# Kernel optimization log

Measured on AMD Instinct MI355X. Metric: run time of the kernel, lower is better.

Reference implementation:

```python
import jax, jax.numpy as jnp
import numpy as np

EMBED_DIM = 1024
NUM_HEADS = 16
HEAD_DIM = EMBED_DIM // NUM_HEADS
SCALE = HEAD_DIM ** -0.5


def setup_inputs() -> dict:
    key = jax.random.key(0)
    ks = jax.random.split(key, 5)
    B, N, D = 2, 2048, EMBED_DIM
    std = D ** -0.5
    x = jax.random.normal(ks[0], (B, N, D), dtype=jnp.float32)
    W_qkv = jax.random.normal(ks[1], (D, 3 * D), dtype=jnp.float32) * std
    b_qkv = jnp.zeros((3 * D,), dtype=jnp.float32)
    W_proj = jax.random.normal(ks[2], (D, D), dtype=jnp.float32) * std
    b_proj = jnp.zeros((D,), dtype=jnp.float32)
    return {"x": x, "W_qkv": W_qkv, "b_qkv": b_qkv, "W_proj": W_proj, "b_proj": b_proj}


def reference(x, W_qkv, b_qkv, W_proj, b_proj):
    B, N, D = x.shape
    H, Hd = NUM_HEADS, HEAD_DIM
    qkv = x @ W_qkv + b_qkv                      # (B, N, 3D)
    qkv = qkv.reshape(B, N, 3, H, Hd)
    q = qkv[:, :, 0].transpose(0, 2, 1, 3)       # (B, H, N, Hd)
    k = qkv[:, :, 1].transpose(0, 2, 1, 3)
    v = qkv[:, :, 2].transpose(0, 2, 1, 3)
    attn = jnp.einsum('bhqd,bhkd->bhqk', q, k) * SCALE  # (B, H, N, N)
    attn = jax.nn.softmax(attn, axis=-1)
    out = jnp.einsum('bhqk,bhkd->bhqd', attn, v)        # (B, H, N, Hd)
    out = out.transpose(0, 2, 1, 3).reshape(B, N, D)
    return out @ W_proj + b_proj
```

## Files before the change

### kernel.cpp

```cpp
#include <hip/hip_runtime.h>
#include <stdint.h>

#define BATCH 2
#define NH 16
#define SEQ 2048
#define DIM 1024
#define HD 64
#define MROWS (BATCH*SEQ)

typedef __attribute__((ext_vector_type(8))) _Float16 f16x8;
typedef __attribute__((ext_vector_type(16))) float f32x16;
typedef __attribute__((ext_vector_type(4))) float f32x4;
typedef __attribute__((ext_vector_type(2))) __fp16 fp16x2;
typedef __attribute__((ext_vector_type(4))) short short4v;
typedef __attribute__((ext_vector_type(2))) unsigned uint2v;

__device__ __forceinline__ short f2h(float f) {
  union { _Float16 h; short s; } u;
  u.h = (_Float16)f;
  return u.s;
}

__device__ __forceinline__ float fast_exp2(float x) {
#if __has_builtin(__builtin_amdgcn_exp2f)
  return __builtin_amdgcn_exp2f(x);
#else
  return exp2f(x);
#endif
}

__device__ __forceinline__ unsigned pk2(float a, float b) {
  union { fp16x2 h; unsigned u; } x;
  x.h = __builtin_amdgcn_cvt_pkrtz(a, b);
  return x.u;
}

__device__ __forceinline__ void perm32swap(unsigned &a, unsigned &b) {
#if __has_builtin(__builtin_amdgcn_permlane32_swap)
  uint2v r = __builtin_amdgcn_permlane32_swap(a, b, false, false);
  a = r[0]; b = r[1];
#else
  unsigned as = (unsigned)__shfl_xor((int)a, 32);
  unsigned bs = (unsigned)__shfl_xor((int)b, 32);
  bool lo = ((threadIdx.x & 63) < 32);
  unsigned na = lo ? a : bs;
  unsigned nb = lo ? as : b;
  a = na; b = nb;
#endif
}

__device__ __forceinline__ void async_load16(const void* g, void* l) {
  __builtin_amdgcn_global_load_lds((const __attribute__((address_space(1))) void*)g,
                                   (__attribute__((address_space(3))) void*)l, 16, 0, 0);
}

__global__ __launch_bounds__(256) void k_cvt(const float* __restrict__ in,
                                             short* __restrict__ out, int n4) {
  int i = blockIdx.x * 256 + threadIdx.x;
  if (i >= n4) return;
  float4 v = ((const float4*)in)[i];
  short4v o;
  o[0] = f2h(v.x); o[1] = f2h(v.y); o[2] = f2h(v.z); o[3] = f2h(v.w);
  ((short4v*)out)[i] = o;
}

__global__ __launch_bounds__(256) void k_transpose(const float* __restrict__ in,
                                                   short* __restrict__ out,
                                                   int K, int N) {
  __shared__ float t[32][33];
  int n0 = blockIdx.x * 32, k0 = blockIdx.y * 32;
  int tx = threadIdx.x, ty = threadIdx.y;
  #pragma unroll
  for (int i = 0; i < 32; i += 8)
    t[ty + i][tx] = in[(size_t)(k0 + ty + i) * N + (n0 + tx)];
  __syncthreads();
  #pragma unroll
  for (int i = 0; i < 32; i += 8)
    out[(size_t)(n0 + ty + i) * K + (k0 + tx)] = f2h(t[tx][ty + i]);
}

template <int MODE, int BM>
__global__ __launch_bounds__(256) void k_gemm_bt(
    const short* __restrict__ A, const short* __restrict__ Bt,
    const float* __restrict__ bias,
    short* __restrict__ Qd, short* __restrict__ Kd, short* __restrict__ Vtd,
    float* __restrict__ Cf, int Ncols, int Kdim) {
  constexpr int BN = 128, BK = 64;
  constexpr int RI = BM / 32;
  __shared__ short Al[2][BM * BK];
  __shared__ short Bl[2][BN * BK];
  const int tid = threadIdx.x;
  const int lane = tid & 63;
  const int wid = tid >> 6;
  const int wr = wid >> 1, wc = wid & 1;
  const int lin = blockIdx.y * (int)gridDim.x + blockIdx.x;
  const int xcd = lin & 7, loc = lin >> 3;
  int bx, by;
  if (MODE == 0) { bx = (xcd & 1) * 12 + loc % 12; by = (xcd >> 1) * 8 + loc / 12; }
  else           { bx = loc % 8;                   by = xcd * 8 + loc / 8; }
  const int m0 = by * BM, n0 = bx * BN;
  const int l15 = lane & 15, lk = (lane >> 4) * 8;

  f32x4 acc[RI][4] = {};

  auto stage = [&](int kt, int buf) {
    int k0 = kt * BK;
    #pragma unroll
    for (int i2 = 0; i2 < BM / 32; i2++) {
      int c = i2 * 256 + tid;
      int r = c >> 3, cs = (c & 7) * 8;
      async_load16(A + (size_t)(m0 + r) * Kdim + k0 + (cs ^ ((r & 7) * 8)),
                   &Al[buf][c * 8]);
    }
    #pragma unroll
    for (int i2 = 0; i2 < 4; i2++) {
      int c = i2 * 256 + tid;
      int r = c >> 3, cs = (c & 7) * 8;
      async_load16(Bt + (size_t)(n0 + r) * Kdim + k0 + (cs ^ ((r & 7) * 8)),
                   &Bl[buf][c * 8]);
    }
  };

  auto compute = [&](int buf) {
    f16x8 af[2][RI], bfr[2][4];
    #pragma unroll
    for (int kk = 0; kk < 2; kk++) {
      #pragma unroll
      for (int i = 0; i < RI; i++) {
        int row = wr * (BM / 2) + i * 16 + l15;
        af[kk][i] = *(const f16x8*)&Al[buf][row * 64 + ((kk * 32 + lk) ^ ((row & 7) * 8))];
      }
      #pragma unroll
      for (int j = 0; j < 4; j++) {
        int row = wc * 64 + j * 16 + l15;
        bfr[kk][j] = *(const f16x8*)&Bl[buf][row * 64 + ((kk * 32 + lk) ^ ((row & 7) * 8))];
      }
    }
    __builtin_amdgcn_s_setprio(1);
    #pragma unroll
    for (int i = 0; i < RI; i++)
      #pragma unroll
      for (int j = 0; j < 4; j++) {
        acc[i][j] = __builtin_amdgcn_mfma_f32_16x16x32_f16(af[0][i], bfr[0][j], acc[i][j], 0, 0, 0);
        acc[i][j] = __builtin_amdgcn_mfma_f32_16x16x32_f16(af[1][i], bfr[1][j], acc[i][j], 0, 0, 0);
      }
    __builtin_amdgcn_s_setprio(0);
  };

  stage(0, 0);
  const int NT = Kdim / BK;
  for (int t = 0; t < NT; t++) {
    int cur = t & 1;
    if (t + 1 < NT) {
      stage(t + 1, cur ^ 1);
      if constexpr (BM == 128) asm volatile("s_waitcnt vmcnt(8)" ::: "memory");
      else                     asm volatile("s_waitcnt vmcnt(6)" ::: "memory");
    } else {
      asm volatile("s_waitcnt vmcnt(0)" ::: "memory");
    }
    __builtin_amdgcn_s_barrier();
    __builtin_amdgcn_sched_barrier(0);
    compute(cur);
    __builtin_amdgcn_sched_barrier(0);
    __builtin_amdgcn_s_barrier();
  }

  const int rl = (lane >> 4) * 4;
  if (MODE == 0) {
    #pragma unroll
    for (int j = 0; j < 4; j++) {
      int col = n0 + wc * 64 + j * 16 + l15;
      float bv = bias[col];
      int sec = col >> 10;
      int cc = col & 1023;
      int h = cc >> 6, hd = cc & 63;
      float mul = (sec == 0) ? (0.125f * 1.44269504088896f) : 1.0f;
      #pragma unroll
      for (int i = 0; i < RI; i++) {
        int rowb = m0 + wr * (BM / 2) + i * 16 + rl;
        #pragma unroll
        for (int r = 0; r < 4; r++) {
          int row = rowb + r;
          int b = row >> 11, nr = row & 2047;
          short v = f2h((acc[i][j][r] + bv) * mul);
          size_t bh = (size_t)(b * NH + h);
          size_t base2 = bh * (size_t)(SEQ * HD);
          if (sec == 0) {
            Qd[base2 + (size_t)nr * HD + hd] = v;
          } else if (sec == 1) {
            Kd[base2 + (size_t)(((nr >> 5) * 4 + (hd >> 4)) * 512 +
                                (((hd >> 3) & 1) * 32 + (nr & 31)) * 8 + (hd & 7))] = v;
          } else {
            Vtd[base2 + (size_t)(((nr >> 4) * 2 + (hd >> 5)) * 512 +
                                 (((nr >> 3) & 1) * 32 + (hd & 31)) * 8 + (nr & 7))] = v;
          }
        }
      }
    }
  } else {
    #pragma unroll
    for (int j = 0; j < 4; j++) {
      int col = n0 + wc * 64 + j * 16 + l15;
      float bv = bias[col];
      #pragma unroll
      for (int i = 0; i < RI; i++) {
        int rowb = m0 + wr * (BM / 2) + i * 16 + rl;
        #pragma unroll
        for (int r = 0; r < 4; r++)
          Cf[(size_t)(rowb + r) * Ncols + col] = acc[i][j][r] + bv;
      }
    }
  }
}

#define QBLK 64
#define NKVT (SEQ / 64)

#define PACK8(sv, R0, lsv, OUT) do {                                        \
    float e0_ = fast_exp2((sv)[R0 + 0]), e1_ = fast_exp2((sv)[R0 + 1]);     \
    float e2_ = fast_exp2((sv)[R0 + 2]), e3_ = fast_exp2((sv)[R0 + 3]);     \
    float e4_ = fast_exp2((sv)[R0 + 4]), e5_ = fast_exp2((sv)[R0 + 5]);     \
    float e6_ = fast_exp2((sv)[R0 + 6]), e7_ = fast_exp2((sv)[R0 + 7]);     \
    lsv += ((e0_ + e1_) + (e2_ + e3_)) + ((e4_ + e5_) + (e6_ + e7_));       \
    unsigned u0_ = pk2(e0_, e1_), u1_ = pk2(e2_, e3_);                      \
    unsigned u2_ = pk2(e4_, e5_), u3_ = pk2(e6_, e7_);                      \
    perm32swap(u0_, u2_);                                                   \
    perm32swap(u1_, u3_);                                                   \
    union { unsigned u[4]; f16x8 v; } W_;                                   \
    W_.u[0] = u0_; W_.u[1] = u1_; W_.u[2] = u2_; W_.u[3] = u3_;             \
    OUT = W_.v;                                                             \
  } while (0)

__global__ __launch_bounds__(256) void k_flash(const short* __restrict__ Qd,
                                               const short* __restrict__ KB,
                                               const short* __restrict__ VB,
                                               short* __restrict__ Od) {
  __shared__ float ob[4096];
  __shared__ float lb[128];
  const int tid = threadIdx.x;
  const int lane = tid & 63;
  const int w = tid >> 6;
  const int wq = w >> 1;
  const int kvh = w & 1;
  const int l31 = lane & 31, lh = lane >> 5;
  const int bh = blockIdx.x;
  const int q0 = blockIdx.y * QBLK + wq * 32;
  const size_t base = (size_t)bh * (size_t)(SEQ * HD);

  f16x8 qf[4];
  #pragma unroll
  for (int ds = 0; ds < 4; ds++)
    qf[ds] = *(const f16x8*)(Qd + base + (size_t)(q0 + l31) * HD + ds * 16 + lh * 8);

  const short* kb = KB + base + kvh * 2048 + (size_t)lane * 8;
  const short* vb = VB + base + kvh * 2048 + (size_t)lane * 8;

  f32x16 o[2] = {};
  float lsum = 0.f;

#define LOADK(t, kf) do {                                                   \
    const short* p_ = kb + (size_t)(t) * 4096;                              \
    kf[0] = *(const f16x8*)(p_);                                            \
    kf[1] = *(const f16x8*)(p_ + 512);                                      \
    kf[2] = *(const f16x8*)(p_ + 1024);                                     \
    kf[3] = *(const f16x8*)(p_ + 1536);                                     \
  } while (0)
#define LOADV(t, vf) do {                                                   \
    const short* p_ = vb + (size_t)(t) * 4096;                              \
    vf[0] = *(const f16x8*)(p_);                               \
    vf[1] = *(const f16x8*)(p_ + 512);                         \
    vf[2] = *(const f16x8*)(p_ + 1024);                        \
    vf[3] = *(const f16x8*)(p_ + 1536);                        \
  } while (0)

  auto compute = [&](const f16x8* kf, const f16x8* vf) {
    f32x16 s = {};
    __builtin_amdgcn_s_setprio(1);
    #pragma unroll
    for (int ds = 0; ds < 4; ds++)
      s = __builtin_amdgcn_mfma_f32_32x32x16_f16(kf[ds], qf[ds], s, 0, 0, 0);
    __builtin_amdgcn_s_setprio(0);
    f16x8 p[2];
    PACK8(s, 0, lsum, p[0]); PACK8(s, 8, lsum, p[1]);
    __builtin_amdgcn_s_setprio(1);
    #pragma unroll
    for (int ks = 0; ks < 2; ks++) {
      o[0] = __builtin_amdgcn_mfma_f32_32x32x16_f16(p[ks], vf[ks * 2 + 0], o[0], 0, 0, 0);
      o[1] = __builtin_amdgcn_mfma_f32_32x32x16_f16(p[ks], vf[ks * 2 + 1], o[1], 0, 0, 0);
    }
    __builtin_amdgcn_s_setprio(0);
  };

  f16x8 kA[4], vA[4], kB_[4], vB_[4];
  LOADK(0, kA); LOADV(0, vA);
  for (int t = 0; t < NKVT; t += 2) {
    if (t + 1 < NKVT) { LOADK(t + 1, kB_); LOADV(t + 1, vB_); }
    compute(kA, vA);
    if (t + 2 < NKVT) { LOADK(t + 2, kA); LOADV(t + 2, vA); }
    if (t + 1 < NKVT) compute(kB_, vB_);
  }
#undef LOADK
#undef LOADV

  if (kvh == 1) {
    #pragma unroll
    for (int hdt = 0; hdt < 2; hdt++)
      #pragma unroll
      for (int rq = 0; rq < 4; rq++) {
        f32x4 v4;
        v4[0] = o[hdt][rq * 4 + 0]; v4[1] = o[hdt][rq * 4 + 1];
        v4[2] = o[hdt][rq * 4 + 2]; v4[3] = o[hdt][rq * 4 + 3];
        *(f32x4*)&ob[wq * 2048 + (hdt * 4 + rq) * 256 + lane * 4] = v4;
      }
    lb[wq * 64 + lane] = lsum;
  }
  __syncthreads();
  if (kvh == 0) {
    #pragma unroll
    for (int hdt = 0; hdt < 2; hdt++)
      #pragma unroll
      for (int rq = 0; rq < 4; rq++) {
        f32x4 v4 = *(const f32x4*)&ob[wq * 2048 + (hdt * 4 + rq) * 256 + lane * 4];
        o[hdt][rq * 4 + 0] += v4[0]; o[hdt][rq * 4 + 1] += v4[1];
        o[hdt][rq * 4 + 2] += v4[2]; o[hdt][rq * 4 + 3] += v4[3];
      }
    lsum += lb[wq * 64 + lane];

    lsum += __shfl_xor(lsum, 32);
    float inv = 1.f / lsum;
    const int b = bh >> 4, h = bh & 15;
    #pragma unroll
    for (int reg = 0; reg < 16; reg++) {
      int qrow = (reg & 3) + 8 * (reg >> 2) + 4 * lh;
      float s = __shfl(inv, qrow);
      size_t r0 = (size_t)(b * SEQ + q0 + qrow) * DIM + h * 64;
      Od[r0 + l31]      = f2h(o[0][reg] * s);
      Od[r0 + 32 + l31] = f2h(o[1][reg] * s);
    }
  }
}

extern "C" void kernel_launch(void* const* d_in, const int* in_sizes, int n_in,
                              void* d_out, int out_size, void* d_ws, size_t ws_size,
                              hipStream_t stream) {
  const float* x     = (const float*)d_in[0];
  const float* Wqkv  = (const float*)d_in[1];
  const float* bqkv  = (const float*)d_in[2];
  const float* Wproj = (const float*)d_in[3];
  const float* bproj = (const float*)d_in[4];
  float* out = (float*)d_out;

  char* ws = (char*)d_ws;
  short* x_h    = (short*)(ws);
  short* Wqkv_t = (short*)(ws + ((size_t)8  << 20));
  short* Wproj_t= (short*)(ws + ((size_t)14 << 20));
  short* Qd     = (short*)(ws + ((size_t)16 << 20));
  short* Kd     = (short*)(ws + ((size_t)24 << 20));
  short* Vtd    = (short*)(ws + ((size_t)32 << 20));
  short* Od     = (short*)(ws + ((size_t)40 << 20));

  k_cvt<<<(MROWS * DIM / 4 + 255) / 256, 256, 0, stream>>>(x, x_h, MROWS * DIM / 4);
  dim3 tb(32, 8);
  k_transpose<<<dim3(3 * DIM / 32, DIM / 32), tb, 0, stream>>>(Wqkv, Wqkv_t, DIM, 3 * DIM);
  k_transpose<<<dim3(DIM / 32, DIM / 32), tb, 0, stream>>>(Wproj, Wproj_t, DIM, DIM);
  k_gemm_bt<0, 128><<<dim3(3 * DIM / 128, MROWS / 128), 256, 0, stream>>>(
      x_h, Wqkv_t, bqkv, Qd, Kd, Vtd, nullptr, 3 * DIM, DIM);
  k_flash<<<dim3(BATCH * NH, SEQ / QBLK), 256, 0, stream>>>(Qd, Kd, Vtd, Od);
  k_gemm_bt<1, 64><<<dim3(DIM / 128, MROWS / 64), 256, 0, stream>>>(
      Od, Wproj_t, bproj, nullptr, nullptr, nullptr, out, DIM, DIM);
}
```

Measured before the change: 130.6 us.

## Split KV range across four waves per 32-query block in flash kernel

Each block now processes 32 queries instead of 64, and its four waves each handle a contiguous quarter of the key/value sequence rather than a 2x2 query/KV-half split. Partial outputs and row sums are merged with a two-stage reduction through shared memory. This doubles the block count and halves each wave's serial loop length, at the cost of each block re-reading the full K/V, so total K/V traffic doubles, and of extra barriers in the reduction.

```diff
diff --git a/kernel.cpp b/kernel.cpp
--- a/kernel.cpp
+++ b/kernel.cpp
@@ -213,8 +213,8 @@
   }
 }
 
-#define QBLK 64
-#define NKVT (SEQ / 64)
+#define QBLK 32
+#define NSTEPS 16
 
 #define PACK8(sv, R0, lsv, OUT) do {                                        \
     float e0_ = fast_exp2((sv)[R0 + 0]), e1_ = fast_exp2((sv)[R0 + 1]);     \
@@ -231,6 +231,13 @@
     OUT = W_.v;                                                             \
   } while (0)
 
+#define LOADH(pt, fr) do {                                                  \
+    fr[0] = *(const f16x8*)(pt);                                            \
+    fr[1] = *(const f16x8*)((pt) + 512);                                    \
+    fr[2] = *(const f16x8*)((pt) + 1024);                                   \
+    fr[3] = *(const f16x8*)((pt) + 1536);                                   \
+  } while (0)
+
 __global__ __launch_bounds__(256) void k_flash(const short* __restrict__ Qd,
                                                const short* __restrict__ KB,
                                                const short* __restrict__ VB,
@@ -240,11 +247,9 @@
   const int tid = threadIdx.x;
   const int lane = tid & 63;
   const int w = tid >> 6;
-  const int wq = w >> 1;
-  const int kvh = w & 1;
   const int l31 = lane & 31, lh = lane >> 5;
   const int bh = blockIdx.x;
-  const int q0 = blockIdx.y * QBLK + wq * 32;
+  const int q0 = blockIdx.y * QBLK;
   const size_t base = (size_t)bh * (size_t)(SEQ * HD);
 
   f16x8 qf[4];
@@ -252,26 +257,11 @@
   for (int ds = 0; ds < 4; ds++)
     qf[ds] = *(const f16x8*)(Qd + base + (size_t)(q0 + l31) * HD + ds * 16 + lh * 8);
 
-  const short* kb = KB + base + kvh * 2048 + (size_t)lane * 8;
-  const short* vb = VB + base + kvh * 2048 + (size_t)lane * 8;
+  const short* kp = KB + base + (size_t)(w * NSTEPS) * 2048 + (size_t)lane * 8;
+  const short* vp = VB + base + (size_t)(w * NSTEPS) * 2048 + (size_t)lane * 8;
 
   f32x16 o[2] = {};
   float lsum = 0.f;
-
-#define LOADK(t, kf) do {                                                   \
-    const short* p_ = kb + (size_t)(t) * 4096;                              \
-    kf[0] = *(const f16x8*)(p_);                                            \
-    kf[1] = *(const f16x8*)(p_ + 512);                                      \
-    kf[2] = *(const f16x8*)(p_ + 1024);                                     \
-    kf[3] = *(const f16x8*)(p_ + 1536);                                     \
-  } while (0)
-#define LOADV(t, vf) do {                                                   \
-    const short* p_ = vb + (size_t)(t) * 4096;                              \
-    vf[0] = *(const f16x8*)(p_);                               \
-    vf[1] = *(const f16x8*)(p_ + 512);                         \
-    vf[2] = *(const f16x8*)(p_ + 1024);                        \
-    vf[3] = *(const f16x8*)(p_ + 1536);                        \
-  } while (0)
 
   auto compute = [&](const f16x8* kf, const f16x8* vf) {
     f32x16 s = {};
@@ -292,17 +282,18 @@
   };
 
   f16x8 kA[4], vA[4], kB_[4], vB_[4];
-  LOADK(0, kA); LOADV(0, vA);
-  for (int t = 0; t < NKVT; t += 2) {
-    if (t + 1 < NKVT) { LOADK(t + 1, kB_); LOADV(t + 1, vB_); }
+  LOADH(kp, kA); LOADH(vp, vA);
+  for (int t = 0; t < NSTEPS; t += 2) {
+    if (t + 1 < NSTEPS) { LOADH(kp + 2048, kB_); LOADH(vp + 2048, vB_); }
     compute(kA, vA);
-    if (t + 2 < NKVT) { LOADK(t + 2, kA); LOADV(t + 2, vA); }
-    if (t + 1 < NKVT) compute(kB_, vB_);
-  }
-#undef LOADK
-#undef LOADV
-
-  if (kvh == 1) {
+    kp += 4096; vp += 4096;
+    if (t + 2 < NSTEPS) { LOADH(kp, kA); LOADH(vp, vA); }
+    if (t + 1 < NSTEPS) compute(kB_, vB_);
+  }
+#undef LOADH
+
+  __syncthreads();
+  if (w >= 2) {
     #pragma unroll
     for (int hdt = 0; hdt < 2; hdt++)
       #pragma unroll
@@ -310,21 +301,46 @@
         f32x4 v4;
         v4[0] = o[hdt][rq * 4 + 0]; v4[1] = o[hdt][rq * 4 + 1];
         v4[2] = o[hdt][rq * 4 + 2]; v4[3] = o[hdt][rq * 4 + 3];
-        *(f32x4*)&ob[wq * 2048 + (hdt * 4 + rq) * 256 + lane * 4] = v4;
-      }
-    lb[wq * 64 + lane] = lsum;
-  }
-  __syncthreads();
-  if (kvh == 0) {
+        *(f32x4*)&ob[(w - 2) * 2048 + (hdt * 4 + rq) * 256 + lane * 4] = v4;
+      }
+    lb[(w - 2) * 64 + lane] = lsum;
+  }
+  __syncthreads();
+  if (w < 2) {
     #pragma unroll
     for (int hdt = 0; hdt < 2; hdt++)
       #pragma unroll
       for (int rq = 0; rq < 4; rq++) {
-        f32x4 v4 = *(const f32x4*)&ob[wq * 2048 + (hdt * 4 + rq) * 256 + lane * 4];
+        f32x4 v4 = *(const f32x4*)&ob[w * 2048 + (hdt * 4 + rq) * 256 + lane * 4];
         o[hdt][rq * 4 + 0] += v4[0]; o[hdt][rq * 4 + 1] += v4[1];
         o[hdt][rq * 4 + 2] += v4[2]; o[hdt][rq * 4 + 3] += v4[3];
       }
-    lsum += lb[wq * 64 + lane];
+    lsum += lb[w * 64 + lane];
+  }
+  __syncthreads();
+  if (w == 1) {
+    #pragma unroll
+    for (int hdt = 0; hdt < 2; hdt++)
+      #pragma unroll
+      for (int rq = 0; rq < 4; rq++) {
+        f32x4 v4;
+        v4[0] = o[hdt][rq * 4 + 0]; v4[1] = o[hdt][rq * 4 + 1];
+        v4[2] = o[hdt][rq * 4 + 2]; v4[3] = o[hdt][rq * 4 + 3];
+        *(f32x4*)&ob[(hdt * 4 + rq) * 256 + lane * 4] = v4;
+      }
+    lb[lane] = lsum;
+  }
+  __syncthreads();
+  if (w == 0) {
+    #pragma unroll
+    for (int hdt = 0; hdt < 2; hdt++)
+      #pragma unroll
+      for (int rq = 0; rq < 4; rq++) {
+        f32x4 v4 = *(const f32x4*)&ob[(hdt * 4 + rq) * 256 + lane * 4];
+        o[hdt][rq * 4 + 0] += v4[0]; o[hdt][rq * 4 + 1] += v4[1];
+        o[hdt][rq * 4 + 2] += v4[2]; o[hdt][rq * 4 + 3] += v4[3];
+      }
+    lsum += lb[lane];
 
     lsum += __shfl_xor(lsum, 32);
     float inv = 1.f / lsum;
```

Result: slower. 135.6 us (+3.8%).
